# Kernel tuning notes

Measured on AMD Instinct MI355X. Metric: run time of the kernel, lower is better.

Reference implementation:

```python
import jax, jax.numpy as jnp
import numpy as np

B, S_F, S_H, S_W = 1, 4, 32, 32
S = S_F * S_H * S_W            # 4096 video tokens
DIM, HEADS = 1536, 12
HD = DIM // HEADS              # 128
EPS = 1e-6


def _rope_angles(max_pos, dim_half):
    inv = 1.0 / (10000.0 ** (np.arange(dim_half, dtype=np.float32) / dim_half))
    return (np.arange(max_pos, dtype=np.float32)[:, None] * inv[None, :]).astype(np.float32)


def setup_inputs():
    key = jax.random.key(0)
    ks = jax.random.split(key, 6)
    w = lambda k: jax.random.normal(k, (DIM, DIM), jnp.float32) * (DIM ** -0.5)
    c = HD // 2
    f0, f1 = c - 2 * (c // 3), c // 3   # 22, 21 (Wan rope split for F/H/W)
    freqs = jnp.asarray(np.concatenate(
        [_rope_angles(1024, f0), _rope_angles(1024, f1), _rope_angles(1024, f1)], axis=1))
    return dict(
        x=jax.random.normal(ks[0], (B, S, DIM), jnp.float32),
        seq_lens=jnp.full((B,), S, jnp.int32),
        grid_sizes=jnp.array([[S_F, S_H, S_W]], jnp.int32),
        freqs=freqs,
        t=500,
        Wq=w(ks[1]), bq=jnp.zeros((DIM,), jnp.float32),
        Wk=w(ks[2]), bk=jnp.zeros((DIM,), jnp.float32),
        Wv=w(ks[3]), bv=jnp.zeros((DIM,), jnp.float32),
        Wo=w(ks[4]), bo=jnp.zeros((DIM,), jnp.float32),
        gq=jnp.ones((DIM,), jnp.float32),
        gk=jnp.ones((DIM,), jnp.float32),
    )


def _rmsnorm(x, g):
    return x * jax.lax.rsqrt(jnp.mean(x * x, axis=-1, keepdims=True) + EPS) * g


def _rope_apply(x, cos, sin):
    # x: [B,S,n,d]; cos/sin: [S, d//2]; rotate interleaved (even, odd) pairs
    b, s, n, d = x.shape
    xr = x.reshape(b, s, n, d // 2, 2)
    xe, xo = xr[..., 0], xr[..., 1]
    c = cos[None, :, None, :]
    sn = sin[None, :, None, :]
    return jnp.stack([xe * c - xo * sn, xe * sn + xo * c], axis=-1).reshape(b, s, n, d)


def _rope_tables(grid_sizes, freqs):
    F, H, W = [int(v) for v in np.asarray(grid_sizes)[0]]
    c = HD // 2
    f0, f1 = c - 2 * (c // 3), c // 3
    ang = jnp.concatenate([
        jnp.broadcast_to(freqs[:F, :f0][:, None, None, :], (F, H, W, f0)),
        jnp.broadcast_to(freqs[:H, f0:f0 + f1][None, :, None, :], (F, H, W, f1)),
        jnp.broadcast_to(freqs[:W, f0 + f1:][None, None, :, :], (F, H, W, f1)),
    ], axis=-1).reshape(F * H * W, c)  # [S, d//2]
    return jnp.cos(ang), jnp.sin(ang)


def reference(x, seq_lens, grid_sizes, freqs, t, Wq, bq, Wk, bk, Wv, bv, Wo, bo, gq, gk):
    b, s = x.shape[:2]
    cos, sin = _rope_tables(grid_sizes, freqs)

    q = _rmsnorm(x @ Wq.T + bq, gq).reshape(b, s, HEADS, HD)
    k = _rmsnorm(x @ Wk.T + bk, gk).reshape(b, s, HEADS, HD)
    v = (x @ Wv.T + bv).reshape(b, s, HEADS, HD)
    q = _rope_apply(q, cos, sin)
    k = _rope_apply(k, cos, sin)

    scores = jnp.einsum('bqhd,bkhd->bhqk', q, k) * (HD ** -0.5)  # [B,H,S,S]
    kmask = jnp.arange(s)[None, :] < seq_lens[:, None]           # varlen key mask
    scores = jnp.where(kmask[:, None, None, :], scores, -jnp.inf)
    attn = jax.nn.softmax(scores, axis=-1)
    out = jnp.einsum('bhqk,bkhd->bqhd', attn, v).reshape(b, s, DIM)
    return out @ Wo.T + bo
```

## Files before the change

kernel.cpp:

```cpp
#include <hip/hip_runtime.h>
#include <hip/hip_bf16.h>

#define S 4096
#define DIM 1536
#define HEADS 12
#define HD 128
#define CHALF 64
#define NQKV 4608

typedef unsigned short u16;
typedef unsigned int u32;
typedef __attribute__((ext_vector_type(8))) short bf16x8;
typedef __attribute__((ext_vector_type(4))) float f32x4;
typedef __attribute__((ext_vector_type(16))) float f32x16;

__device__ __forceinline__ u16 f2b(float f) {
    u32 u = __float_as_uint(f);
    u32 r = (u + 0x7fffu + ((u >> 16) & 1u)) >> 16;
    return (u16)r;
}
__device__ __forceinline__ float b2f(u16 b) {
    return __uint_as_float(((u32)b) << 16);
}
__device__ __forceinline__ u32 pack2(float a, float b) {
    u32 lo = (__float_as_uint(a) + 0x8000u) >> 16;
    u32 hi = (__float_as_uint(b) + 0x8000u) & 0xffff0000u;
    return lo | hi;
}
__device__ __forceinline__ void gld_lds16(const u16* g, u16* l) {
    __builtin_amdgcn_global_load_lds((const __attribute__((address_space(1))) void*)g,
                                     (__attribute__((address_space(3))) void*)l, 16, 0, 0);
}

__global__ void k_cvt_all(const float4* __restrict__ x, const float4* __restrict__ wq,
                          const float4* __restrict__ wk, const float4* __restrict__ wv,
                          const float4* __restrict__ wo,
                          ushort4* __restrict__ xb, ushort4* __restrict__ wqkv,
                          ushort4* __restrict__ wob,
                          const float* __restrict__ freqs, const int* __restrict__ grid_sizes,
                          float* __restrict__ cosT, float* __restrict__ sinT) {
    const int N4X = S * DIM / 4, N4W = DIM * DIM / 4;
    const int NCVT = N4X + 4 * N4W;
    int i = blockIdx.x * 256 + threadIdx.x;
    if (i < NCVT) {
        const float4* src; ushort4* dst; int off;
        if (i < N4X) { src = x; dst = xb; off = i; }
        else {
            int j = i - N4X;
            int w = j / N4W; off = j - w * N4W;
            if (w == 0)      { src = wq; dst = wqkv; }
            else if (w == 1) { src = wk; dst = wqkv + N4W; }
            else if (w == 2) { src = wv; dst = wqkv + 2 * N4W; }
            else             { src = wo; dst = wob; }
        }
        float4 v = src[off];
        ushort4 o;
        o.x = f2b(v.x); o.y = f2b(v.y); o.z = f2b(v.z); o.w = f2b(v.w);
        dst[off] = o;
    } else {
        int idx = i - NCVT;
        int s = idx >> 6;
        int ii = idx & 63;
        int H = grid_sizes[1], W = grid_sizes[2];
        int hw = H * W;
        int f = s / hw;
        int rem = s - f * hw;
        int h = rem / W;
        int w = rem - h * W;
        const int f0 = 22, f1 = 21;
        int pos = (ii < f0) ? f : ((ii < f0 + f1) ? h : w);
        float ang = freqs[pos * CHALF + ii];
        cosT[idx] = cosf(ang);
        sinT[idx] = sinf(ang);
    }
}

template<int TN, int OUT_BF16, int QKV>
__global__ __launch_bounds__(256, 2) void k_gemm(const u16* __restrict__ A, const u16* __restrict__ W,
                                                 const float* __restrict__ b0, const float* __restrict__ b1,
                                                 const float* __restrict__ b2,
                                                 void* __restrict__ Cout, int N, int K, int ldc) {
    __shared__ u16 As[128 * 64];
    __shared__ u16 Bs[TN * 64];
    int tid = threadIdx.x;
    int lane = tid & 63, wave = tid >> 6;
    int l31 = lane & 31, hi = lane >> 5;
    int rowBase = blockIdx.y * 128;
    int colBase = blockIdx.x * TN;

    int srow = lane >> 3;
    int scol = (((lane & 7) ^ (srow & 7)) << 3);

    constexpr int MI = (TN == 128) ? 2 : 1;
    int rw = (TN == 128) ? ((wave >> 1) * 64) : (wave * 32);
    int cw = (TN == 128) ? ((wave & 1) * 64) : 0;
    int lx = l31 & 7;

    f32x16 acc[MI][2] = {};

    for (int kb = 0; kb < K; kb += 64) {
        __syncthreads();
        {
#pragma unroll
            for (int it = 0; it < 4; it++) {
                int rb = wave * 32 + it * 8;
                gld_lds16(A + (size_t)(rowBase + rb + srow) * K + kb + scol, As + rb * 64);
            }
#pragma unroll
            for (int it = 0; it < (TN == 128 ? 4 : 2); it++) {
                int rb = wave * (TN == 128 ? 32 : 16) + it * 8;
                gld_lds16(W + (size_t)(colBase + rb + srow) * K + kb + scol, Bs + rb * 64);
            }
        }
        __syncthreads();

#pragma unroll
        for (int kk = 0; kk < 4; kk++) {
            int chk = ((kk * 2 + hi) ^ lx) << 3;
            bf16x8 af[MI], bf[2];
#pragma unroll
            for (int mi = 0; mi < MI; mi++)
                af[mi] = *(const bf16x8*)(As + (rw + mi * 32 + l31) * 64 + chk);
#pragma unroll
            for (int ni = 0; ni < 2; ni++)
                bf[ni] = *(const bf16x8*)(Bs + (cw + ni * 32 + l31) * 64 + chk);
#pragma unroll
            for (int mi = 0; mi < MI; mi++)
#pragma unroll
                for (int ni = 0; ni < 2; ni++)
                    acc[mi][ni] = __builtin_amdgcn_mfma_f32_32x32x16_bf16(af[mi], bf[ni], acc[mi][ni], 0, 0, 0);
        }
    }

#pragma unroll
    for (int mi = 0; mi < MI; mi++) {
#pragma unroll
        for (int ni = 0; ni < 2; ni++) {
            int col = colBase + cw + ni * 32 + l31;
            float bv;
            if (QKV) {
                int third = colBase / DIM;
                const float* bp = (third == 0) ? b0 : ((third == 1) ? b1 : b2);
                bv = bp[col - third * DIM];
            } else {
                bv = b0[col];
            }
#pragma unroll
            for (int g = 0; g < 16; g++) {
                int row = rowBase + rw + mi * 32 + (g & 3) + 8 * (g >> 2) + 4 * hi;
                float v = acc[mi][ni][g] + bv;
                if (OUT_BF16)
                    ((u16*)Cout)[(size_t)row * ldc + col] = f2b(v);
                else
                    ((float*)Cout)[(size_t)row * ldc + col] = v;
            }
        }
    }
}

__global__ __launch_bounds__(256) void k_normrope(u16* __restrict__ qkvp, const float* __restrict__ gq,
                                                  const float* __restrict__ gk,
                                                  const float* __restrict__ cosT, const float* __restrict__ sinT,
                                                  float qscale) {
    int s = blockIdx.x;
    int which = blockIdx.y;
    const float* g = which ? gk : gq;
    float scale = which ? 1.0f : qscale;
    int tid = threadIdx.x;
    int lane = tid & 63, wave = tid >> 6;
    u32* row = (u32*)(qkvp + (size_t)s * NQKV + which * DIM);

    int w0 = tid, w1 = tid + 256, w2 = tid + 512;
    u32 p0 = row[w0], p1 = row[w1], p2 = row[w2];
    float e0 = b2f(p0 & 0xffff), o0 = b2f(p0 >> 16);
    float e1 = b2f(p1 & 0xffff), o1 = b2f(p1 >> 16);
    float e2 = b2f(p2 & 0xffff), o2 = b2f(p2 >> 16);
    float ss = e0 * e0 + o0 * o0 + e1 * e1 + o1 * o1 + e2 * e2 + o2 * o2;

    __shared__ float wsum[4];
    for (int off = 32; off; off >>= 1) ss += __shfl_down(ss, off);
    if (lane == 0) wsum[wave] = ss;
    __syncthreads();
    float tot = wsum[0] + wsum[1] + wsum[2] + wsum[3];
    float r = rsqrtf(tot * (1.0f / DIM) + 1e-6f) * scale;

    const float* cr = cosT + (size_t)s * CHALF;
    const float* sr = sinT + (size_t)s * CHALF;
#pragma unroll
    for (int j = 0; j < 3; j++) {
        int p = (j == 0) ? w0 : (j == 1) ? w1 : w2;
        float e = (j == 0) ? e0 : (j == 1) ? e1 : e2;
        float o = (j == 0) ? o0 : (j == 1) ? o1 : o2;
        int i = p & 63;
        float c = cr[i], sn = sr[i];
        e = e * r * g[2 * p];
        o = o * r * g[2 * p + 1];
        float ne = e * c - o * sn;
        float no = e * sn + o * c;
        row[p] = (u32)f2b(ne) | ((u32)f2b(no) << 16);
    }
}

__global__ void k_transpose(const u16* __restrict__ src, u16* __restrict__ dst) {
    __shared__ u16 t[32][33];
    int bx = blockIdx.x;
    int by = blockIdx.y;
    int tx = threadIdx.x, ty = threadIdx.y;
#pragma unroll
    for (int i = 0; i < 4; i++)
        t[ty + i * 8][tx] = src[(size_t)(by * 32 + ty + i * 8) * NQKV + bx * 32 + tx];
    __syncthreads();
    int txp = (tx & ~12) | ((tx & 4) << 1) | ((tx & 8) >> 1);
#pragma unroll
    for (int i = 0; i < 4; i++)
        dst[(size_t)(bx * 32 + ty + i * 8) * S + by * 32 + txp] = t[tx][ty + i * 8];
}

__global__ __launch_bounds__(256, 3) void k_attn(const u16* __restrict__ qkv, const u16* __restrict__ vt,
                                                 u16* __restrict__ O0, u16* __restrict__ O1,
                                                 float* __restrict__ lT,
                                                 const int* __restrict__ seq_lens) {
    int bx = blockIdx.x;
    int xcd = bx & 7, slot = bx >> 3;
    int hp = xcd * 3 + (slot >> 5);
    int h = (hp >= HEADS) ? hp - HEADS : hp;
    int p = (hp >= HEADS) ? 1 : 0;
    int q0 = (slot & 31) * 128;
    int kh0 = p * (S / 2);
    int tid = threadIdx.x;
    int lane = tid & 63, wave = tid >> 6;
    int l31 = lane & 31, hi = lane >> 5;
    int seqlen = seq_lens[0];
    u16* Op = p ? O1 : O0;

    __shared__ u16 Ks[64 * 136];
    __shared__ u16 Vs[128 * 88];

    int qrow = q0 + wave * 32 + l31;
    bf16x8 qf[8];
#pragma unroll
    for (int c = 0; c < 8; c++)
        qf[c] = *(const bf16x8*)(qkv + (size_t)qrow * NQKV + h * HD + c * 16 + hi * 8);

    f32x16 o_acc[4] = {};
    float lsum = 0.f;

    for (int kt = 0; kt < S / 2; kt += 64) {
        int kbase = kh0 + kt;
        __syncthreads();
        {
            int r = tid >> 2, cc = (tid & 3) * 32;
#pragma unroll
            for (int u = 0; u < 4; u++) {
                uint4 kv = *(const uint4*)(qkv + (size_t)(kbase + r) * NQKV + DIM + h * HD + cc + u * 8);
                *(uint4*)(Ks + r * 136 + cc + u * 8) = kv;
            }
            int dr = tid >> 3, dc = (tid & 7) * 8;
#pragma unroll
            for (int it = 0; it < 4; it++)
                *(uint4*)(Vs + (dr + it * 32) * 88 + dc) =
                    *(const uint4*)(vt + (size_t)(h * HD + dr + it * 32) * S + kbase + dc);
        }
        __syncthreads();

        f32x16 sc0 = {}, sc1 = {};
#pragma unroll
        for (int c = 0; c < 8; c++) {
            bf16x8 kf0 = *(const bf16x8*)(Ks + l31 * 136 + c * 16 + hi * 8);
            bf16x8 kf1 = *(const bf16x8*)(Ks + (32 + l31) * 136 + c * 16 + hi * 8);
            sc0 = __builtin_amdgcn_mfma_f32_32x32x16_bf16(kf0, qf[c], sc0, 0, 0, 0);
            sc1 = __builtin_amdgcn_mfma_f32_32x32x16_bf16(kf1, qf[c], sc1, 0, 0, 0);
        }

        bool tail = (kbase + 64 > seqlen);
        bf16x8 pfrag[4];
#pragma unroll
        for (int b = 0; b < 2; b++) {
            f32x16 s16 = b ? sc1 : sc0;
            u32 pk[4][2];
            if (!tail) {
#pragma unroll
                for (int g = 0; g < 4; g++) {
                    float e0 = __builtin_amdgcn_exp2f(s16[4 * g + 0]);
                    float e1 = __builtin_amdgcn_exp2f(s16[4 * g + 1]);
                    float e2 = __builtin_amdgcn_exp2f(s16[4 * g + 2]);
                    float e3 = __builtin_amdgcn_exp2f(s16[4 * g + 3]);
                    lsum += (e0 + e1) + (e2 + e3);
                    pk[g][0] = pack2(e0, e1);
                    pk[g][1] = pack2(e2, e3);
                }
            } else {
#pragma unroll
                for (int g = 0; g < 4; g++) {
                    float e[4];
#pragma unroll
                    for (int r = 0; r < 4; r++) {
                        int key = kbase + b * 32 + r + 8 * g + 4 * hi;
                        float v = __builtin_amdgcn_exp2f(s16[4 * g + r]);
                        e[r] = (key < seqlen) ? v : 0.f;
                        lsum += e[r];
                    }
                    pk[g][0] = pack2(e[0], e[1]);
                    pk[g][1] = pack2(e[2], e[3]);
                }
            }
            union { u32 u[4]; bf16x8 v; } c0v, c1v;
            c0v.u[0] = pk[0][0]; c0v.u[1] = pk[0][1]; c0v.u[2] = pk[1][0]; c0v.u[3] = pk[1][1];
            c1v.u[0] = pk[2][0]; c1v.u[1] = pk[2][1]; c1v.u[2] = pk[3][0]; c1v.u[3] = pk[3][1];
            pfrag[b * 2 + 0] = c0v.v;
            pfrag[b * 2 + 1] = c1v.v;
        }

#pragma unroll
        for (int db = 0; db < 4; db++) {
#pragma unroll
            for (int c4 = 0; c4 < 4; c4++) {
                bf16x8 vf = *(const bf16x8*)(Vs + (db * 32 + l31) * 88 + c4 * 16 + hi * 8);
                o_acc[db] = __builtin_amdgcn_mfma_f32_32x32x16_bf16(vf, pfrag[c4], o_acc[db], 0, 0, 0);
            }
        }
    }

    float l_all = lsum + __shfl_xor(lsum, 32);
    float linv = 1.0f / l_all;
#pragma unroll
    for (int db = 0; db < 4; db++) {
#pragma unroll
        for (int g = 0; g < 4; g++) {
            int d0 = db * 32 + 8 * g + 4 * hi;
            u16 o4[4];
#pragma unroll
            for (int r = 0; r < 4; r++)
                o4[r] = f2b(o_acc[db][4 * g + r] * linv);
            *(uint2*)(Op + (size_t)qrow * DIM + h * HD + d0) = *(const uint2*)o4;
        }
    }
    if (!hi) lT[((size_t)p * HEADS + h) * S + qrow] = l_all;
}

__global__ __launch_bounds__(384) void k_combine(u16* __restrict__ O0, const u16* __restrict__ O1,
                                                 const float* __restrict__ lT) {
    int q = blockIdx.x;
    int tid = threadIdx.x;
    int h = tid >> 5;
    size_t base = (size_t)q * DIM + tid * 4;
    float l0 = lT[(size_t)h * S + q];
    float l1 = lT[(size_t)(HEADS + h) * S + q];
    float inv = 1.0f / (l0 + l1);
    float c0 = l0 * inv, c1 = l1 * inv;
    uint2 u0 = *(const uint2*)(O0 + base);
    uint2 u1 = *(const uint2*)(O1 + base);
    const u16* a = (const u16*)&u0;
    const u16* b = (const u16*)&u1;
    u16 o[4];
#pragma unroll
    for (int i = 0; i < 4; i++)
        o[i] = f2b(c0 * b2f(a[i]) + c1 * b2f(b[i]));
    *(uint2*)(O0 + base) = *(uint2*)o;
}

extern "C" void kernel_launch(void* const* d_in, const int* in_sizes, int n_in,
                              void* d_out, int out_size, void* d_ws, size_t ws_size,
                              hipStream_t stream) {
    const float* x = (const float*)d_in[0];
    const int* seq_lens = (const int*)d_in[1];
    const int* grid_sizes = (const int*)d_in[2];
    const float* freqs = (const float*)d_in[3];
    const float* Wq = (const float*)d_in[5];
    const float* bq = (const float*)d_in[6];
    const float* Wk = (const float*)d_in[7];
    const float* bk = (const float*)d_in[8];
    const float* Wv = (const float*)d_in[9];
    const float* bv = (const float*)d_in[10];
    const float* Wo = (const float*)d_in[11];
    const float* bo = (const float*)d_in[12];
    const float* gq = (const float*)d_in[13];
    const float* gk = (const float*)d_in[14];
    float* out = (float*)d_out;

    char* w = (char*)d_ws;
    u16* xb    = (u16*)w; w += (size_t)S * DIM * 2;
    u16* qkv   = (u16*)w; w += (size_t)S * NQKV * 2;
    u16* Wqkvb = (u16*)w; w += (size_t)3 * DIM * DIM * 2;
    u16* Wob   = (u16*)w; w += (size_t)DIM * DIM * 2;
    u16* ab    = (u16*)w; w += (size_t)S * DIM * 2;
    u16* O1    = (u16*)w; w += (size_t)S * DIM * 2;
    float* cosT = (float*)w; w += (size_t)S * CHALF * 4;
    float* sinT = (float*)w; w += (size_t)S * CHALF * 4;
    float* lT  = (float*)w; w += (size_t)2 * HEADS * S * 4;
    u16* vt = Wqkvb;

    const float qscale = 0.08838834764831845f * 1.44269504088896341f;

    const int N4X = S * DIM / 4, N4W = DIM * DIM / 4;
    const int NCVT = N4X + 4 * N4W;
    const int NTAB = S * CHALF;
    k_cvt_all<<<(NCVT + NTAB) / 256, 256, 0, stream>>>(
        (const float4*)x, (const float4*)Wq, (const float4*)Wk, (const float4*)Wv, (const float4*)Wo,
        (ushort4*)xb, (ushort4*)Wqkvb, (ushort4*)Wob,
        freqs, grid_sizes, cosT, sinT);

    k_gemm<128, 1, 1><<<dim3(NQKV / 128, S / 128), 256, 0, stream>>>(
        xb, Wqkvb, bq, bk, bv, qkv, NQKV, DIM, NQKV);

    k_normrope<<<dim3(S, 2), 256, 0, stream>>>(qkv, gq, gk, cosT, sinT, qscale);

    k_transpose<<<dim3(DIM / 32, S / 32), dim3(32, 8), 0, stream>>>(qkv + 2 * DIM, vt);

    k_attn<<<dim3(768), 256, 0, stream>>>(qkv, vt, ab, O1, lT, seq_lens);

    k_combine<<<S, 384, 0, stream>>>(ab, O1, lT);

    k_gemm<64, 0, 0><<<dim3(DIM / 64, S / 128), 256, 0, stream>>>(
        ab, Wob, bo, bo, bo, out, DIM, DIM, DIM);
}
```

Measured before the change: 372.8 us.

## Fuse split-KV combine into output projection GEMM A-tile load

Removes the separate combine kernel. The Wo GEMM now loads both partial attention outputs and the log-sum terms, merges them in registers, and writes the bf16 A tile straight into LDS, so the intermediate round trip through global memory goes away. The GEMM template is split into specialized QKV and Wo kernels, and launch bounds change from 2 to 3 blocks per CU. In exchange, the A tile is now loaded synchronously with no async LDS path, and the combine work is repeated for every column block of the Wo GEMM.

```diff
diff --git a/kernel.cpp b/kernel.cpp
--- a/kernel.cpp
+++ b/kernel.cpp
@@ -75,57 +75,49 @@
     }
 }
 
-template<int TN, int OUT_BF16, int QKV>
-__global__ __launch_bounds__(256, 2) void k_gemm(const u16* __restrict__ A, const u16* __restrict__ W,
-                                                 const float* __restrict__ b0, const float* __restrict__ b1,
-                                                 const float* __restrict__ b2,
-                                                 void* __restrict__ Cout, int N, int K, int ldc) {
+__global__ __launch_bounds__(256, 3) void k_gemm_qkv(const u16* __restrict__ A, const u16* __restrict__ W,
+                                                     const float* __restrict__ b0, const float* __restrict__ b1,
+                                                     const float* __restrict__ b2,
+                                                     u16* __restrict__ Cout) {
     __shared__ u16 As[128 * 64];
-    __shared__ u16 Bs[TN * 64];
+    __shared__ u16 Bs[128 * 64];
     int tid = threadIdx.x;
     int lane = tid & 63, wave = tid >> 6;
     int l31 = lane & 31, hi = lane >> 5;
     int rowBase = blockIdx.y * 128;
-    int colBase = blockIdx.x * TN;
+    int colBase = blockIdx.x * 128;
 
     int srow = lane >> 3;
     int scol = (((lane & 7) ^ (srow & 7)) << 3);
 
-    constexpr int MI = (TN == 128) ? 2 : 1;
-    int rw = (TN == 128) ? ((wave >> 1) * 64) : (wave * 32);
-    int cw = (TN == 128) ? ((wave & 1) * 64) : 0;
+    int rw = (wave >> 1) * 64;
+    int cw = (wave & 1) * 64;
     int lx = l31 & 7;
 
-    f32x16 acc[MI][2] = {};
-
-    for (int kb = 0; kb < K; kb += 64) {
-        __syncthreads();
-        {
-#pragma unroll
-            for (int it = 0; it < 4; it++) {
-                int rb = wave * 32 + it * 8;
-                gld_lds16(A + (size_t)(rowBase + rb + srow) * K + kb + scol, As + rb * 64);
-            }
-#pragma unroll
-            for (int it = 0; it < (TN == 128 ? 4 : 2); it++) {
-                int rb = wave * (TN == 128 ? 32 : 16) + it * 8;
-                gld_lds16(W + (size_t)(colBase + rb + srow) * K + kb + scol, Bs + rb * 64);
-            }
+    f32x16 acc[2][2] = {};
+
+    for (int kb = 0; kb < DIM; kb += 64) {
+        __syncthreads();
+#pragma unroll
+        for (int it = 0; it < 4; it++) {
+            int rb = wave * 32 + it * 8;
+            gld_lds16(A + (size_t)(rowBase + rb + srow) * DIM + kb + scol, As + rb * 64);
+            gld_lds16(W + (size_t)(colBase + rb + srow) * DIM + kb + scol, Bs + rb * 64);
         }
         __syncthreads();
 
 #pragma unroll
         for (int kk = 0; kk < 4; kk++) {
             int chk = ((kk * 2 + hi) ^ lx) << 3;
-            bf16x8 af[MI], bf[2];
-#pragma unroll
-            for (int mi = 0; mi < MI; mi++)
+            bf16x8 af[2], bf[2];
+#pragma unroll
+            for (int mi = 0; mi < 2; mi++)
                 af[mi] = *(const bf16x8*)(As + (rw + mi * 32 + l31) * 64 + chk);
 #pragma unroll
             for (int ni = 0; ni < 2; ni++)
                 bf[ni] = *(const bf16x8*)(Bs + (cw + ni * 32 + l31) * 64 + chk);
 #pragma unroll
-            for (int mi = 0; mi < MI; mi++)
+            for (int mi = 0; mi < 2; mi++)
 #pragma unroll
                 for (int ni = 0; ni < 2; ni++)
                     acc[mi][ni] = __builtin_amdgcn_mfma_f32_32x32x16_bf16(af[mi], bf[ni], acc[mi][ni], 0, 0, 0);
@@ -133,27 +125,94 @@
     }
 
 #pragma unroll
-    for (int mi = 0; mi < MI; mi++) {
+    for (int mi = 0; mi < 2; mi++) {
 #pragma unroll
         for (int ni = 0; ni < 2; ni++) {
             int col = colBase + cw + ni * 32 + l31;
-            float bv;
-            if (QKV) {
-                int third = colBase / DIM;
-                const float* bp = (third == 0) ? b0 : ((third == 1) ? b1 : b2);
-                bv = bp[col - third * DIM];
-            } else {
-                bv = b0[col];
-            }
+            int third = colBase / DIM;
+            const float* bp = (third == 0) ? b0 : ((third == 1) ? b1 : b2);
+            float bv = bp[col - third * DIM];
 #pragma unroll
             for (int g = 0; g < 16; g++) {
                 int row = rowBase + rw + mi * 32 + (g & 3) + 8 * (g >> 2) + 4 * hi;
-                float v = acc[mi][ni][g] + bv;
-                if (OUT_BF16)
-                    ((u16*)Cout)[(size_t)row * ldc + col] = f2b(v);
-                else
-                    ((float*)Cout)[(size_t)row * ldc + col] = v;
+                Cout[(size_t)row * NQKV + col] = f2b(acc[mi][ni][g] + bv);
             }
+        }
+    }
+}
+
+__global__ __launch_bounds__(256, 3) void k_gemm_wo(const u16* __restrict__ O0, const u16* __restrict__ O1,
+                                                    const float* __restrict__ lT,
+                                                    const u16* __restrict__ W, const float* __restrict__ bias,
+                                                    float* __restrict__ Cout) {
+    __shared__ u16 As[128 * 64];
+    __shared__ u16 Bs[64 * 64];
+    int tid = threadIdx.x;
+    int lane = tid & 63, wave = tid >> 6;
+    int l31 = lane & 31, hi = lane >> 5;
+    int rowBase = blockIdx.y * 128;
+    int colBase = blockIdx.x * 64;
+
+    int srow = lane >> 3;
+    int scol = (((lane & 7) ^ (srow & 7)) << 3);
+
+    int arow = tid >> 1, ahalf = tid & 1;
+    int aqrow = rowBase + arow;
+
+    int rw = wave * 32;
+    int lx = l31 & 7;
+
+    f32x16 acc[2] = {};
+
+    for (int kb = 0; kb < DIM; kb += 64) {
+        int h = kb >> 7;
+        float l0 = lT[(size_t)h * S + aqrow];
+        float l1 = lT[(size_t)(HEADS + h) * S + aqrow];
+        float inv = 1.0f / (l0 + l1);
+        float c0 = l0 * inv, c1 = l1 * inv;
+        __syncthreads();
+#pragma unroll
+        for (int it = 0; it < 2; it++) {
+            int rb = wave * 16 + it * 8;
+            gld_lds16(W + (size_t)(colBase + rb + srow) * DIM + kb + scol, Bs + rb * 64);
+        }
+#pragma unroll
+        for (int jj = 0; jj < 4; jj++) {
+            int j = ahalf * 4 + jj;
+            uint4 u0 = *(const uint4*)(O0 + (size_t)aqrow * DIM + kb + j * 8);
+            uint4 u1 = *(const uint4*)(O1 + (size_t)aqrow * DIM + kb + j * 8);
+            const u16* a = (const u16*)&u0;
+            const u16* b = (const u16*)&u1;
+            u32 w4[4];
+#pragma unroll
+            for (int t = 0; t < 4; t++) {
+                float v0 = c0 * b2f(a[2 * t]) + c1 * b2f(b[2 * t]);
+                float v1 = c0 * b2f(a[2 * t + 1]) + c1 * b2f(b[2 * t + 1]);
+                w4[t] = (u32)f2b(v0) | ((u32)f2b(v1) << 16);
+            }
+            *(uint4*)(As + arow * 64 + ((j ^ (arow & 7)) << 3)) = *(uint4*)w4;
+        }
+        __syncthreads();
+
+#pragma unroll
+        for (int kk = 0; kk < 4; kk++) {
+            int chk = ((kk * 2 + hi) ^ lx) << 3;
+            bf16x8 af = *(const bf16x8*)(As + (rw + l31) * 64 + chk);
+            bf16x8 bf0 = *(const bf16x8*)(Bs + l31 * 64 + chk);
+            bf16x8 bf1 = *(const bf16x8*)(Bs + (32 + l31) * 64 + chk);
+            acc[0] = __builtin_amdgcn_mfma_f32_32x32x16_bf16(af, bf0, acc[0], 0, 0, 0);
+            acc[1] = __builtin_amdgcn_mfma_f32_32x32x16_bf16(af, bf1, acc[1], 0, 0, 0);
+        }
+    }
+
+#pragma unroll
+    for (int ni = 0; ni < 2; ni++) {
+        int col = colBase + ni * 32 + l31;
+        float bv = bias[col];
+#pragma unroll
+        for (int g = 0; g < 16; g++) {
+            int row = rowBase + rw + (g & 3) + 8 * (g >> 2) + 4 * hi;
+            Cout[(size_t)row * DIM + col] = acc[ni][g] + bv;
         }
     }
 }
@@ -336,27 +395,6 @@
         }
     }
     if (!hi) lT[((size_t)p * HEADS + h) * S + qrow] = l_all;
-}
-
-__global__ __launch_bounds__(384) void k_combine(u16* __restrict__ O0, const u16* __restrict__ O1,
-                                                 const float* __restrict__ lT) {
-    int q = blockIdx.x;
-    int tid = threadIdx.x;
-    int h = tid >> 5;
-    size_t base = (size_t)q * DIM + tid * 4;
-    float l0 = lT[(size_t)h * S + q];
-    float l1 = lT[(size_t)(HEADS + h) * S + q];
-    float inv = 1.0f / (l0 + l1);
-    float c0 = l0 * inv, c1 = l1 * inv;
-    uint2 u0 = *(const uint2*)(O0 + base);
-    uint2 u1 = *(const uint2*)(O1 + base);
-    const u16* a = (const u16*)&u0;
-    const u16* b = (const u16*)&u1;
-    u16 o[4];
-#pragma unroll
-    for (int i = 0; i < 4; i++)
-        o[i] = f2b(c0 * b2f(a[i]) + c1 * b2f(b[i]));
-    *(uint2*)(O0 + base) = *(uint2*)o;
 }
 
 extern "C" void kernel_launch(void* const* d_in, const int* in_sizes, int n_in,
@@ -400,8 +438,8 @@
         (ushort4*)xb, (ushort4*)Wqkvb, (ushort4*)Wob,
         freqs, grid_sizes, cosT, sinT);
 
-    k_gemm<128, 1, 1><<<dim3(NQKV / 128, S / 128), 256, 0, stream>>>(
-        xb, Wqkvb, bq, bk, bv, qkv, NQKV, DIM, NQKV);
+    k_gemm_qkv<<<dim3(NQKV / 128, S / 128), 256, 0, stream>>>(
+        xb, Wqkvb, bq, bk, bv, qkv);
 
     k_normrope<<<dim3(S, 2), 256, 0, stream>>>(qkv, gq, gk, cosT, sinT, qscale);
 
@@ -409,8 +447,6 @@
 
     k_attn<<<dim3(768), 256, 0, stream>>>(qkv, vt, ab, O1, lT, seq_lens);
 
-    k_combine<<<S, 384, 0, stream>>>(ab, O1, lT);
-
-    k_gemm<64, 0, 0><<<dim3(DIM / 64, S / 128), 256, 0, stream>>>(
-        ab, Wob, bo, bo, bo, out, DIM, DIM, DIM);
-}
+    k_gemm_wo<<<dim3(DIM / 64, S / 128), 256, 0, stream>>>(
+        ab, O1, lT, Wob, bo, out);
+}
```

Measured after the change: 416.3 us. 1.12x slower.
